# Performance work log

Measured on AMD Instinct MI355X. Metric: run time of the kernel, lower is better.

## Reference

```python
import jax, jax.numpy as jnp
import numpy as np

SEQ, B, H, NP, HN = 2048, 2, 2048, 16, 128
SCALE = 1.0 / 11.313708498984761  # 1/sqrt(128), hardcoded in the source baddbmm


def setup_inputs() -> dict:
    key = jax.random.key(0)
    k1, k2, k3 = jax.random.split(key, 3)
    return {
        "hidden_states": jax.random.normal(k1, (SEQ, B, H), dtype=jnp.float32),
        "w_qkv": jax.random.normal(k2, (3 * H, H), dtype=jnp.float32) * 0.02,
        "w_out": jax.random.normal(k3, (H, H), dtype=jnp.float32) * 0.02,
    }


def reference(hidden_states, w_qkv, w_out):
    s, b, h = hidden_states.shape
    # QKV projection (column-parallel linear, no bias): [s, b, 3h]
    qkv = hidden_states @ w_qkv.T
    # [s, b, np, 3*hn] then split (num_query_groups == num_heads)
    qkv = qkv.reshape(s, b, NP, 3 * HN)
    q, k, v = qkv[..., :HN], qkv[..., HN:2 * HN], qkv[..., 2 * HN:]
    # baddbmm QK^T with alpha = 1/sqrt(128): scores [b, np, sq, sk]
    scores = jnp.einsum("sbnh,tbnh->bnst", q, k) * SCALE
    # scale_t == 1 then plain softmax (fallback path; no mask applied)
    prob = jax.nn.softmax(scores, axis=-1)
    # context: bmm(prob, V) -> [sq, b, np, hn] -> [sq, b, h]
    ctx = jnp.einsum("bnst,tbnh->sbnh", prob, v).reshape(s, b, h)
    # row-parallel output linear (no bias)
    return ctx @ w_out.T
```

## Files before the change

### kernel.cpp

```cpp
#include <hip/hip_runtime.h>
#include <stdint.h>

#define SEQ 2048
#define BATCH 2
#define HID 2048
#define NHEADS 16
#define HDIM 128
#define QKV_LD 6144
#define SCALE_F 0.08838834764831845f
#define LOG2E_F 1.4426950408889634f

typedef unsigned short u16;
using bf16x8 = __attribute__((ext_vector_type(8))) short;
using f32x4  = __attribute__((ext_vector_type(4))) float;

__device__ inline u16 f2bf(float f) {
  union { float f; uint32_t u; } c; c.f = f;
  uint32_t u = c.u;
  uint32_t r = (u + 0x7fffu + ((u >> 16) & 1u)) >> 16;
  return (u16)r;
}

__device__ inline void gl_lds16(const u16* g, u16* l) {
  __builtin_amdgcn_global_load_lds((const __attribute__((address_space(1))) void*)g,
                                   (__attribute__((address_space(3))) void*)l,
                                   16, 0, 0);
}

__global__ void cvt_all(const float* __restrict__ hs, const float* __restrict__ wqkv,
                        const float* __restrict__ wout, u16* __restrict__ ws_out) {
  int i = blockIdx.x * blockDim.x + threadIdx.x;
  const float* src;
  int j;
  float sc = 1.0f;
  if (i < 2097152) { src = hs; j = i; }
  else if (i < 5242880) {
    j = i - 2097152; src = wqkv;
    const int f = j >> 9;
    if ((f % 384) < 128) sc = SCALE_F;
  } else { j = i - 5242880; src = wout; }
  float4 v = ((const float4*)src)[j];
  ushort4 o;
  o.x = f2bf(v.x * sc); o.y = f2bf(v.y * sc); o.z = f2bf(v.z * sc); o.w = f2bf(v.w * sc);
  ((ushort4*)ws_out)[i] = o;
}

template<int MODE>
__global__ __launch_bounds__(256)
void gemm_bt(const u16* __restrict__ A, const u16* __restrict__ Bw,
             void* __restrict__ Cout, u16* __restrict__ vt, int M, int N, int K) {
  __shared__ __align__(16) u16 As[128 * 64];
  __shared__ __align__(16) u16 Bs[128 * 64];
  const int bm = blockIdx.x, bn = blockIdx.y;
  const int tid = threadIdx.x;
  const int wave = tid >> 6, lane = tid & 63;
  const int quad = lane >> 4, l16 = lane & 15;
  const int wm = (wave >> 1) * 64, wn = (wave & 1) * 64;
  f32x4 acc[4][4] = {};

  const u16* Ablk = A + (size_t)(bm * 128) * K;
  const u16* Bblk = Bw + (size_t)(bn * 128) * K;

  for (int k0 = 0; k0 < K; k0 += 64) {
    __syncthreads();
    #pragma unroll
    for (int p = 0; p < 4; ++p) {
      int j = p * 256 + tid;
      int r = j >> 3, cs = j & 7, c = cs ^ (r & 7);
      gl_lds16(Ablk + (size_t)r * K + k0 + c * 8, As + (p * 256 + wave * 64) * 8);
      gl_lds16(Bblk + (size_t)r * K + k0 + c * 8, Bs + (p * 256 + wave * 64) * 8);
    }
    __syncthreads();
    #pragma unroll
    for (int ks = 0; ks < 2; ++ks) {
      bf16x8 af[4], bfr[4];
      #pragma unroll
      for (int mt = 0; mt < 4; ++mt) {
        int row = wm + mt * 16 + l16;
        int cc = (ks * 4 + quad) ^ (row & 7);
        af[mt] = *(const bf16x8*)&As[(row * 8 + cc) * 8];
      }
      #pragma unroll
      for (int nt = 0; nt < 4; ++nt) {
        int row = wn + nt * 16 + l16;
        int cc = (ks * 4 + quad) ^ (row & 7);
        bfr[nt] = *(const bf16x8*)&Bs[(row * 8 + cc) * 8];
      }
      #pragma unroll
      for (int mt = 0; mt < 4; ++mt)
        #pragma unroll
        for (int nt = 0; nt < 4; ++nt)
          acc[mt][nt] = __builtin_amdgcn_mfma_f32_16x16x32_bf16(af[mt], bfr[nt], acc[mt][nt], 0, 0, 0);
    }
  }

  if (MODE == 1 && (bn % 3) == 2) {
    const int h = bn / 3;
    u16* vt0 = vt + ((size_t)h * HDIM) * SEQ;
    u16* vt1 = vt + ((size_t)(NHEADS + h) * HDIM) * SEQ;
    #pragma unroll
    for (int mt = 0; mt < 4; ++mt)
      #pragma unroll
      for (int nt = 0; nt < 4; ++nt) {
        const int hd = wn + nt * 16 + l16;
        const int s0 = (bm * 128 + wm + mt * 16 + quad * 4) >> 1;
        uint32_t w0 = (uint32_t)f2bf(acc[mt][nt][0]) | ((uint32_t)f2bf(acc[mt][nt][2]) << 16);
        uint32_t w1 = (uint32_t)f2bf(acc[mt][nt][1]) | ((uint32_t)f2bf(acc[mt][nt][3]) << 16);
        *(uint32_t*)&vt0[(size_t)hd * SEQ + s0] = w0;
        *(uint32_t*)&vt1[(size_t)hd * SEQ + s0] = w1;
      }
    return;
  }

  #pragma unroll
  for (int mt = 0; mt < 4; ++mt)
    #pragma unroll
    for (int nt = 0; nt < 4; ++nt)
      #pragma unroll
      for (int r = 0; r < 4; ++r) {
        int row = bm * 128 + wm + mt * 16 + quad * 4 + r;
        int col = bn * 128 + wn + nt * 16 + l16;
        float v = acc[mt][nt][r];
        if (MODE == 1) ((u16*)Cout)[(size_t)row * N + col] = f2bf(v);
        else           ((float*)Cout)[(size_t)row * N + col] = v;
      }
}

__global__ __launch_bounds__(512, 2)
void attn(const u16* __restrict__ qkv, const u16* __restrict__ vt_g, u16* __restrict__ ctx) {
  const int qt = blockIdx.x, head = blockIdx.y, b = blockIdx.z;
  const int q0 = qt * 256;
  __shared__ __align__(16) u16 Ks[64 * 128];
  __shared__ __align__(16) u16 Vt[144 * 64];
  __shared__ __align__(16) u16 PsT[256 * 64];
  const int tid = threadIdx.x;
  const int wave = tid >> 6, lane = tid & 63;
  const int quad = lane >> 4, l16 = lane & 15;

  const u16* qkv_bh = qkv + (size_t)b * QKV_LD + head * 384;
  const u16* vt = vt_g + (size_t)(b * NHEADS + head) * HDIM * SEQ;

  if (tid < 128) {
    const int row = 128 + (tid >> 3), c = tid & 7;
    const u16 v = (row == 128) ? (u16)0x3F80 : (u16)0;
    ushort4 q4; q4.x = v; q4.y = v; q4.z = v; q4.w = v;
    *(ushort4*)&Vt[(row * 8 + c) * 8] = q4;
    *(ushort4*)&Vt[(row * 8 + c) * 8 + 4] = q4;
  }

  bf16x8 qf[2][4];
  #pragma unroll
  for (int h = 0; h < 4; ++h) {
    __syncthreads();
    #pragma unroll
    for (int p = 0; p < 2; ++p) {
      int j = p * 512 + tid;
      int r = j >> 4, cs = j & 15, c = cs ^ (r & 7);
      gl_lds16(qkv_bh + (size_t)(q0 + h * 64 + r) * (BATCH * QKV_LD) + c * 8,
               Ks + (p * 512 + wave * 64) * 8);
    }
    __syncthreads();
    if ((wave >> 1) == h) {
      #pragma unroll
      for (int nt = 0; nt < 2; ++nt)
        #pragma unroll
        for (int ks = 0; ks < 4; ++ks) {
          int row = (wave & 1) * 32 + nt * 16 + l16;
          int cc = (ks * 4 + quad) ^ (row & 7);
          qf[nt][ks] = *(const bf16x8*)&Ks[(row * 16 + cc) * 8];
        }
    }
  }

  f32x4 ot[9][2] = {};

  for (int kt = 0; kt < SEQ; kt += 64) {
    __syncthreads();
    #pragma unroll
    for (int p = 0; p < 2; ++p) {
      int j = p * 512 + tid;
      int r = j >> 4, cs = j & 15, c = cs ^ (r & 7);
      gl_lds16(qkv_bh + (size_t)(kt + r) * (BATCH * QKV_LD) + 128 + c * 8,
               Ks + (p * 512 + wave * 64) * 8);
    }
    #pragma unroll
    for (int p = 0; p < 2; ++p) {
      int j = p * 512 + tid;
      int hd = j >> 3, cs = j & 7, c = cs ^ (hd & 7);
      gl_lds16(vt + (size_t)hd * SEQ + kt + c * 8,
               Vt + (p * 512 + wave * 64) * 8);
    }
    __syncthreads();

    f32x4 st[4][2] = {};
    #pragma unroll
    for (int ks = 0; ks < 4; ++ks) {
      bf16x8 kf[4];
      #pragma unroll
      for (int mt = 0; mt < 4; ++mt) {
        int key = mt * 16 + l16;
        int cc = (ks * 4 + quad) ^ (key & 7);
        kf[mt] = *(const bf16x8*)&Ks[(key * 16 + cc) * 8];
      }
      #pragma unroll
      for (int mt = 0; mt < 4; ++mt)
        #pragma unroll
        for (int nt = 0; nt < 2; ++nt)
          st[mt][nt] = __builtin_amdgcn_mfma_f32_16x16x32_bf16(kf[mt], qf[nt][ks], st[mt][nt], 0, 0, 0);
    }

    #pragma unroll
    for (int mt = 0; mt < 4; ++mt)
      #pragma unroll
      for (int nt = 0; nt < 2; ++nt) {
        ushort4 pk;
        union { float f; uint32_t u; } cv;
        cv.f = __builtin_amdgcn_exp2f(st[mt][nt][0] * LOG2E_F); pk.x = (u16)(cv.u >> 16);
        cv.f = __builtin_amdgcn_exp2f(st[mt][nt][1] * LOG2E_F); pk.y = (u16)(cv.u >> 16);
        cv.f = __builtin_amdgcn_exp2f(st[mt][nt][2] * LOG2E_F); pk.z = (u16)(cv.u >> 16);
        cv.f = __builtin_amdgcn_exp2f(st[mt][nt][3] * LOG2E_F); pk.w = (u16)(cv.u >> 16);
        const int q = wave * 32 + nt * 16 + l16;
        const int kc = mt * 2 + (quad >> 1);
        *(ushort4*)&PsT[q * 64 + ((kc ^ (l16 & 7)) * 8 + (quad & 1) * 4)] = pk;
      }

    #pragma unroll
    for (int ks = 0; ks < 2; ++ks) {
      bf16x8 pf[2], vf[9];
      #pragma unroll
      for (int nt = 0; nt < 2; ++nt) {
        const int q = wave * 32 + nt * 16 + l16;
        const int cc = (ks * 4 + quad) ^ (l16 & 7);
        pf[nt] = *(const bf16x8*)&PsT[q * 64 + cc * 8];
      }
      #pragma unroll
      for (int mt = 0; mt < 9; ++mt) {
        const int hd = mt * 16 + l16;
        const int cc = (ks * 4 + quad) ^ (hd & 7);
        vf[mt] = *(const bf16x8*)&Vt[(hd * 8 + cc) * 8];
      }
      #pragma unroll
      for (int mt = 0; mt < 9; ++mt)
        #pragma unroll
        for (int nt = 0; nt < 2; ++nt)
          ot[mt][nt] = __builtin_amdgcn_mfma_f32_16x16x32_bf16(vf[mt], pf[nt], ot[mt][nt], 0, 0, 0);
    }
  }

  #pragma unroll
  for (int nt = 0; nt < 2; ++nt) {
    const float lv = __shfl(ot[8][nt][0], l16);
    const float inv_l = 1.0f / lv;
    const int s = q0 + wave * 32 + nt * 16 + l16;
    u16* dst = ctx + ((size_t)s * BATCH + b) * HID + head * HDIM;
    #pragma unroll
    for (int mt = 0; mt < 8; ++mt) {
      ushort4 w;
      w.x = f2bf(ot[mt][nt][0] * inv_l);
      w.y = f2bf(ot[mt][nt][1] * inv_l);
      w.z = f2bf(ot[mt][nt][2] * inv_l);
      w.w = f2bf(ot[mt][nt][3] * inv_l);
      *(ushort4*)&dst[mt * 16 + quad * 4] = w;
    }
  }
}

extern "C" void kernel_launch(void* const* d_in, const int* in_sizes, int n_in,
                              void* d_out, int out_size, void* d_ws, size_t ws_size,
                              hipStream_t stream) {
  const float* hs   = (const float*)d_in[0];
  const float* wqkv = (const float*)d_in[1];
  const float* wout = (const float*)d_in[2];
  float* out = (float*)d_out;
  char* ws = (char*)d_ws;

  u16* hs_bf   = (u16*)(ws);
  u16* wqkv_bf = (u16*)(ws + 16777216);
  u16* wout_bf = (u16*)(ws + 41943040);
  u16* qkv_bf  = (u16*)(ws + 50331648);
  u16* vt_bf   = (u16*)(ws + 100663296);
  u16* ctx_bf  = hs_bf;

  cvt_all<<<24576, 256, 0, stream>>>(hs, wqkv, wout, (u16*)ws);

  gemm_bt<1><<<dim3(32, 48), 256, 0, stream>>>(hs_bf, wqkv_bf, qkv_bf, vt_bf, 4096, 6144, 2048);

  attn<<<dim3(8, NHEADS, BATCH), 512, 0, stream>>>(qkv_bf, vt_bf, ctx_bf);

  gemm_bt<0><<<dim3(32, 16), 256, 0, stream>>>(ctx_bf, wout_bf, out, nullptr, 4096, 2048, 2048);
}
```

Measured before the change: 382.7 us.

## Triple-buffer GEMM LDS tiles with 128x256 blocks and 512 threads

Rewrites the bf16 GEMM to use 128x256 output tiles with 8 waves and a three-stage LDS ring. Global-to-LDS loads are issued two k-steps ahead and guarded by vmcnt waits, so each iteration needs one barrier instead of two. MFMA priority is raised with s_setprio. The change aims to hide global load latency and improve B-operand reuse. In exchange it uses about 144KB of LDS per block, which limits occupancy, and with half as many blocks per launch it may underfill the CUs.

Result: slower. 410.5 us (+7.3%).

```diff
diff --git a/kernel.cpp b/kernel.cpp
--- a/kernel.cpp
+++ b/kernel.cpp
@@ -45,32 +45,54 @@
   ((ushort4*)ws_out)[i] = o;
 }
 
+__device__ __forceinline__ void stage_tile(const u16* __restrict__ Ablk,
+                                           const u16* __restrict__ Bblk,
+                                           int K, int k0, u16* As, u16* Bs,
+                                           int tid, int wave) {
+  #pragma unroll
+  for (int p = 0; p < 2; ++p) {
+    int j = p * 512 + tid;
+    int r = j >> 3, cs = j & 7, c = cs ^ (r & 7);
+    gl_lds16(Ablk + (size_t)r * K + k0 + c * 8, As + (size_t)(p * 512 + wave * 64) * 8);
+  }
+  #pragma unroll
+  for (int p = 0; p < 4; ++p) {
+    int j = p * 512 + tid;
+    int r = j >> 3, cs = j & 7, c = cs ^ (r & 7);
+    gl_lds16(Bblk + (size_t)r * K + k0 + c * 8, Bs + (size_t)(p * 512 + wave * 64) * 8);
+  }
+}
+
 template<int MODE>
-__global__ __launch_bounds__(256)
+__global__ __launch_bounds__(512)
 void gemm_bt(const u16* __restrict__ A, const u16* __restrict__ Bw,
              void* __restrict__ Cout, u16* __restrict__ vt, int M, int N, int K) {
-  __shared__ __align__(16) u16 As[128 * 64];
-  __shared__ __align__(16) u16 Bs[128 * 64];
+  __shared__ __align__(16) u16 As[3][128 * 64];
+  __shared__ __align__(16) u16 Bs[3][256 * 64];
   const int bm = blockIdx.x, bn = blockIdx.y;
   const int tid = threadIdx.x;
   const int wave = tid >> 6, lane = tid & 63;
   const int quad = lane >> 4, l16 = lane & 15;
-  const int wm = (wave >> 1) * 64, wn = (wave & 1) * 64;
+  const int wm = (wave >> 2) * 64, wn = (wave & 3) * 64;
   f32x4 acc[4][4] = {};
 
   const u16* Ablk = A + (size_t)(bm * 128) * K;
-  const u16* Bblk = Bw + (size_t)(bn * 128) * K;
-
-  for (int k0 = 0; k0 < K; k0 += 64) {
-    __syncthreads();
-    #pragma unroll
-    for (int p = 0; p < 4; ++p) {
-      int j = p * 256 + tid;
-      int r = j >> 3, cs = j & 7, c = cs ^ (r & 7);
-      gl_lds16(Ablk + (size_t)r * K + k0 + c * 8, As + (p * 256 + wave * 64) * 8);
-      gl_lds16(Bblk + (size_t)r * K + k0 + c * 8, Bs + (p * 256 + wave * 64) * 8);
-    }
-    __syncthreads();
+  const u16* Bblk = Bw + (size_t)(bn * 256) * K;
+  const int nt = K >> 6;
+
+  stage_tile(Ablk, Bblk, K, 0,  As[0], Bs[0], tid, wave);
+  stage_tile(Ablk, Bblk, K, 64, As[1], Bs[1], tid, wave);
+  asm volatile("s_waitcnt vmcnt(6)" ::: "memory");
+  __builtin_amdgcn_s_barrier();
+
+  for (int t = 0; t < nt; ++t) {
+    const int cur = t % 3;
+    if (t + 2 < nt) {
+      const int nb = (t + 2) % 3;
+      stage_tile(Ablk, Bblk, K, (t + 2) * 64, As[nb], Bs[nb], tid, wave);
+    }
+    const u16* Asb = As[cur];
+    const u16* Bsb = Bs[cur];
     #pragma unroll
     for (int ks = 0; ks < 2; ++ks) {
       bf16x8 af[4], bfr[4];
@@ -78,51 +100,68 @@
       for (int mt = 0; mt < 4; ++mt) {
         int row = wm + mt * 16 + l16;
         int cc = (ks * 4 + quad) ^ (row & 7);
-        af[mt] = *(const bf16x8*)&As[(row * 8 + cc) * 8];
-      }
-      #pragma unroll
-      for (int nt = 0; nt < 4; ++nt) {
-        int row = wn + nt * 16 + l16;
+        af[mt] = *(const bf16x8*)&Asb[(row * 8 + cc) * 8];
+      }
+      #pragma unroll
+      for (int nt2 = 0; nt2 < 4; ++nt2) {
+        int row = wn + nt2 * 16 + l16;
         int cc = (ks * 4 + quad) ^ (row & 7);
-        bfr[nt] = *(const bf16x8*)&Bs[(row * 8 + cc) * 8];
-      }
+        bfr[nt2] = *(const bf16x8*)&Bsb[(row * 8 + cc) * 8];
+      }
+      __builtin_amdgcn_s_setprio(1);
       #pragma unroll
       for (int mt = 0; mt < 4; ++mt)
         #pragma unroll
-        for (int nt = 0; nt < 4; ++nt)
-          acc[mt][nt] = __builtin_amdgcn_mfma_f32_16x16x32_bf16(af[mt], bfr[nt], acc[mt][nt], 0, 0, 0);
-    }
-  }
-
-  if (MODE == 1 && (bn % 3) == 2) {
-    const int h = bn / 3;
-    u16* vt0 = vt + ((size_t)h * HDIM) * SEQ;
-    u16* vt1 = vt + ((size_t)(NHEADS + h) * HDIM) * SEQ;
+        for (int nt2 = 0; nt2 < 4; ++nt2)
+          acc[mt][nt2] = __builtin_amdgcn_mfma_f32_16x16x32_bf16(af[mt], bfr[nt2], acc[mt][nt2], 0, 0, 0);
+      __builtin_amdgcn_s_setprio(0);
+    }
+    if (t + 2 < nt) asm volatile("s_waitcnt vmcnt(6)" ::: "memory");
+    else            asm volatile("s_waitcnt vmcnt(0)" ::: "memory");
+    __builtin_amdgcn_s_barrier();
+  }
+
+  if (MODE == 1) {
+    #pragma unroll
+    for (int ntf = 0; ntf < 4; ++ntf) {
+      const int coff = wn + ntf * 16;
+      const int g = bn * 2 + (coff >> 7);
+      const int h = g / 3;
+      if ((g % 3) == 2) {
+        const int hd = (coff & 127) + l16;
+        u16* vt0 = vt + ((size_t)h * HDIM) * SEQ;
+        u16* vt1 = vt + ((size_t)(NHEADS + h) * HDIM) * SEQ;
+        #pragma unroll
+        for (int mt = 0; mt < 4; ++mt) {
+          const int s0 = (bm * 128 + wm + mt * 16 + quad * 4) >> 1;
+          uint32_t w0 = (uint32_t)f2bf(acc[mt][ntf][0]) | ((uint32_t)f2bf(acc[mt][ntf][2]) << 16);
+          uint32_t w1 = (uint32_t)f2bf(acc[mt][ntf][1]) | ((uint32_t)f2bf(acc[mt][ntf][3]) << 16);
+          *(uint32_t*)&vt0[(size_t)hd * SEQ + s0] = w0;
+          *(uint32_t*)&vt1[(size_t)hd * SEQ + s0] = w1;
+        }
+      } else {
+        const int col = bn * 256 + coff + l16;
+        #pragma unroll
+        for (int mt = 0; mt < 4; ++mt)
+          #pragma unroll
+          for (int r = 0; r < 4; ++r) {
+            const int row = bm * 128 + wm + mt * 16 + quad * 4 + r;
+            ((u16*)Cout)[(size_t)row * N + col] = f2bf(acc[mt][ntf][r]);
+          }
+      }
+    }
+    return;
+  }
+
+  #pragma unroll
+  for (int ntf = 0; ntf < 4; ++ntf)
     #pragma unroll
     for (int mt = 0; mt < 4; ++mt)
       #pragma unroll
-      for (int nt = 0; nt < 4; ++nt) {
-        const int hd = wn + nt * 16 + l16;
-        const int s0 = (bm * 128 + wm + mt * 16 + quad * 4) >> 1;
-        uint32_t w0 = (uint32_t)f2bf(acc[mt][nt][0]) | ((uint32_t)f2bf(acc[mt][nt][2]) << 16);
-        uint32_t w1 = (uint32_t)f2bf(acc[mt][nt][1]) | ((uint32_t)f2bf(acc[mt][nt][3]) << 16);
-        *(uint32_t*)&vt0[(size_t)hd * SEQ + s0] = w0;
-        *(uint32_t*)&vt1[(size_t)hd * SEQ + s0] = w1;
-      }
-    return;
-  }
-
-  #pragma unroll
-  for (int mt = 0; mt < 4; ++mt)
-    #pragma unroll
-    for (int nt = 0; nt < 4; ++nt)
-      #pragma unroll
       for (int r = 0; r < 4; ++r) {
-        int row = bm * 128 + wm + mt * 16 + quad * 4 + r;
-        int col = bn * 128 + wn + nt * 16 + l16;
-        float v = acc[mt][nt][r];
-        if (MODE == 1) ((u16*)Cout)[(size_t)row * N + col] = f2bf(v);
-        else           ((float*)Cout)[(size_t)row * N + col] = v;
+        const int row = bm * 128 + wm + mt * 16 + quad * 4 + r;
+        const int col = bn * 256 + wn + ntf * 16 + l16;
+        ((float*)Cout)[(size_t)row * N + col] = acc[mt][ntf][r];
       }
 }
 
@@ -283,9 +322,9 @@
 
   cvt_all<<<24576, 256, 0, stream>>>(hs, wqkv, wout, (u16*)ws);
 
-  gemm_bt<1><<<dim3(32, 48), 256, 0, stream>>>(hs_bf, wqkv_bf, qkv_bf, vt_bf, 4096, 6144, 2048);
+  gemm_bt<1><<<dim3(32, 24), 512, 0, stream>>>(hs_bf, wqkv_bf, qkv_bf, vt_bf, 4096, 6144, 2048);
 
   attn<<<dim3(8, NHEADS, BATCH), 512, 0, stream>>>(qkv_bf, vt_bf, ctx_bf);
 
-  gemm_bt<0><<<dim3(32, 16), 256, 0, stream>>>(ctx_bf, wout_bf, out, nullptr, 4096, 2048, 2048);
-}
+  gemm_bt<0><<<dim3(32, 8), 512, 0, stream>>>(ctx_bf, wout_bf, out, nullptr, 4096, 2048, 2048);
+}
```

## Replace QKV GEMM with double-buffered 256x256-tile kernel with interleaved prefetch

Applied to the files above, without the earlier changes.

Adds a dedicated QKV projection kernel that uses 256x256 output tiles with 8 waves, double-buffered LDS filled by direct global-to-LDS loads, and prefetches interleaved with MFMA phases using explicit vmcnt waits, barriers and setprio. The goal is to hide global load latency and raise per-block data reuse compared with the old unpipelined 128x128 kernel. The V-transpose epilogue moves into the new kernel and is resolved per 64-column chunk, and the old MODE 1 path is dropped from gemm_bt. The cost is more LDS (128KB per block) and more registers, which lowers occupancy, plus fragile hand-tuned wait counts.

Result: slower. 429.4 us (+12.2%).

```diff
diff --git a/kernel.cpp b/kernel.cpp
--- a/kernel.cpp
+++ b/kernel.cpp
@@ -45,12 +45,178 @@
   ((ushort4*)ws_out)[i] = o;
 }
 
+#define QK_M 4096
+#define QK_N 6144
+#define QK_K 2048
+#define QK_T (QK_K / 64)
+
+__global__ __launch_bounds__(512, 2)
+void gemm256_qkv(const u16* __restrict__ A, const u16* __restrict__ Bw,
+                 u16* __restrict__ Cout, u16* __restrict__ vt) {
+  __shared__ __align__(16) u16 As[2][16384];
+  __shared__ __align__(16) u16 Bs[2][16384];
+  const int bm = blockIdx.x, bn = blockIdx.y;
+  const int tid = threadIdx.x;
+  const int wave = tid >> 6, lane = tid & 63;
+  const int quad = lane >> 4, l16 = lane & 15;
+  const int wm = (wave >> 2) * 128, wn = (wave & 3) * 64;
+  f32x4 acc[8][4] = {};
+
+  const u16* Ablk = A + (size_t)(bm * 256) * QK_K;
+  const u16* Bblk = Bw + (size_t)(bn * 256) * QK_K;
+
+  auto stageA = [&](int t, int ks, int buf) {
+    #pragma unroll
+    for (int p = 0; p < 2; ++p) {
+      int j = p * 512 + tid;
+      int row = ((j >> 6) << 4) + (j & 15);
+      int c = (j >> 4) & 3;
+      gl_lds16(Ablk + (size_t)row * QK_K + t * 64 + ks * 32 + c * 8,
+               &As[buf][ks * 8192 + (p * 512 + wave * 64) * 8]);
+    }
+  };
+  auto stageB = [&](int t, int ks, int buf) {
+    #pragma unroll
+    for (int p = 0; p < 2; ++p) {
+      int j = p * 512 + tid;
+      int row = ((j >> 6) << 4) + (j & 15);
+      int c = (j >> 4) & 3;
+      gl_lds16(Bblk + (size_t)row * QK_K + t * 64 + ks * 32 + c * 8,
+               &Bs[buf][ks * 8192 + (p * 512 + wave * 64) * 8]);
+    }
+  };
+
+  stageA(0, 0, 0); stageB(0, 0, 0);
+  stageA(0, 1, 0); stageB(0, 1, 0);
+  stageA(1, 0, 1); stageB(1, 0, 1);
+  asm volatile("s_waitcnt vmcnt(8)" ::: "memory");
+  __builtin_amdgcn_s_barrier();
+  __builtin_amdgcn_sched_barrier(0);
+
+  for (int t = 0; t < QK_T; ++t) {
+    const int cb = t & 1;
+    const u16* Ab = &As[cb][0];
+    const u16* Bb = &Bs[cb][0];
+    bf16x8 af[4], bfr[4];
+
+    #pragma unroll
+    for (int mt = 0; mt < 4; ++mt) {
+      int row = wm + mt * 16 + l16;
+      af[mt] = *(const bf16x8*)&Ab[(((row >> 4) << 6) + quad * 16 + (row & 15)) * 8];
+    }
+    #pragma unroll
+    for (int nt = 0; nt < 4; ++nt) {
+      int row = wn + nt * 16 + l16;
+      bfr[nt] = *(const bf16x8*)&Bb[(((row >> 4) << 6) + quad * 16 + (row & 15)) * 8];
+    }
+    if (t + 1 < QK_T) stageA(t + 1, 1, cb ^ 1);
+    __builtin_amdgcn_s_barrier();
+    __builtin_amdgcn_s_setprio(1);
+    #pragma unroll
+    for (int mt = 0; mt < 4; ++mt)
+      #pragma unroll
+      for (int nt = 0; nt < 4; ++nt)
+        acc[mt][nt] = __builtin_amdgcn_mfma_f32_16x16x32_bf16(af[mt], bfr[nt], acc[mt][nt], 0, 0, 0);
+    __builtin_amdgcn_s_setprio(0);
+    __builtin_amdgcn_s_barrier();
+
+    #pragma unroll
+    for (int mt = 0; mt < 4; ++mt) {
+      int row = wm + 64 + mt * 16 + l16;
+      af[mt] = *(const bf16x8*)&Ab[(((row >> 4) << 6) + quad * 16 + (row & 15)) * 8];
+    }
+    if (t + 1 < QK_T) stageB(t + 1, 1, cb ^ 1);
+    __builtin_amdgcn_s_barrier();
+    __builtin_amdgcn_s_setprio(1);
+    #pragma unroll
+    for (int mt = 0; mt < 4; ++mt)
+      #pragma unroll
+      for (int nt = 0; nt < 4; ++nt)
+        acc[4 + mt][nt] = __builtin_amdgcn_mfma_f32_16x16x32_bf16(af[mt], bfr[nt], acc[4 + mt][nt], 0, 0, 0);
+    __builtin_amdgcn_s_setprio(0);
+    if (t < QK_T - 1) asm volatile("s_waitcnt vmcnt(8)" ::: "memory");
+    else              asm volatile("s_waitcnt vmcnt(0)" ::: "memory");
+    __builtin_amdgcn_s_barrier();
+    __builtin_amdgcn_sched_barrier(0);
+
+    #pragma unroll
+    for (int mt = 0; mt < 4; ++mt) {
+      int row = wm + mt * 16 + l16;
+      af[mt] = *(const bf16x8*)&Ab[8192 + (((row >> 4) << 6) + quad * 16 + (row & 15)) * 8];
+    }
+    #pragma unroll
+    for (int nt = 0; nt < 4; ++nt) {
+      int row = wn + nt * 16 + l16;
+      bfr[nt] = *(const bf16x8*)&Bb[8192 + (((row >> 4) << 6) + quad * 16 + (row & 15)) * 8];
+    }
+    if (t + 2 < QK_T) stageA(t + 2, 0, cb);
+    __builtin_amdgcn_s_barrier();
+    __builtin_amdgcn_s_setprio(1);
+    #pragma unroll
+    for (int mt = 0; mt < 4; ++mt)
+      #pragma unroll
+      for (int nt = 0; nt < 4; ++nt)
+        acc[mt][nt] = __builtin_amdgcn_mfma_f32_16x16x32_bf16(af[mt], bfr[nt], acc[mt][nt], 0, 0, 0);
+    __builtin_amdgcn_s_setprio(0);
+    __builtin_amdgcn_s_barrier();
+
+    #pragma unroll
+    for (int mt = 0; mt < 4; ++mt) {
+      int row = wm + 64 + mt * 16 + l16;
+      af[mt] = *(const bf16x8*)&Ab[8192 + (((row >> 4) << 6) + quad * 16 + (row & 15)) * 8];
+    }
+    if (t + 2 < QK_T) stageB(t + 2, 0, cb);
+    __builtin_amdgcn_s_barrier();
+    __builtin_amdgcn_s_setprio(1);
+    #pragma unroll
+    for (int mt = 0; mt < 4; ++mt)
+      #pragma unroll
+      for (int nt = 0; nt < 4; ++nt)
+        acc[4 + mt][nt] = __builtin_amdgcn_mfma_f32_16x16x32_bf16(af[mt], bfr[nt], acc[4 + mt][nt], 0, 0, 0);
+    __builtin_amdgcn_s_setprio(0);
+    if (t < QK_T - 2)       asm volatile("s_waitcnt vmcnt(8)" ::: "memory");
+    else if (t == QK_T - 2) asm volatile("s_waitcnt vmcnt(4)" ::: "memory");
+    else                    asm volatile("s_waitcnt vmcnt(0)" ::: "memory");
+    __builtin_amdgcn_s_barrier();
+    __builtin_amdgcn_sched_barrier(0);
+  }
+
+  #pragma unroll
+  for (int ntf = 0; ntf < 4; ++ntf) {
+    const int coff = wn + ntf * 16;
+    const int g = bn * 2 + (coff >> 7);
+    const int h = g / 3;
+    if ((g % 3) == 2) {
+      const int hd = (coff & 127) + l16;
+      u16* vt0 = vt + ((size_t)h * HDIM) * SEQ;
+      u16* vt1 = vt + ((size_t)(NHEADS + h) * HDIM) * SEQ;
+      #pragma unroll
+      for (int mt = 0; mt < 8; ++mt) {
+        const int s0 = (bm * 256 + wm + mt * 16 + quad * 4) >> 1;
+        uint32_t w0 = (uint32_t)f2bf(acc[mt][ntf][0]) | ((uint32_t)f2bf(acc[mt][ntf][2]) << 16);
+        uint32_t w1 = (uint32_t)f2bf(acc[mt][ntf][1]) | ((uint32_t)f2bf(acc[mt][ntf][3]) << 16);
+        *(uint32_t*)&vt0[(size_t)hd * SEQ + s0] = w0;
+        *(uint32_t*)&vt1[(size_t)hd * SEQ + s0] = w1;
+      }
+    } else {
+      const int col = bn * 256 + coff + l16;
+      #pragma unroll
+      for (int mt = 0; mt < 8; ++mt)
+        #pragma unroll
+        for (int r = 0; r < 4; ++r) {
+          const int row = bm * 256 + wm + mt * 16 + quad * 4 + r;
+          Cout[(size_t)row * QK_N + col] = f2bf(acc[mt][ntf][r]);
+        }
+    }
+  }
+}
+
 template<int MODE>
 __global__ __launch_bounds__(256)
 void gemm_bt(const u16* __restrict__ A, const u16* __restrict__ Bw,
              void* __restrict__ Cout, u16* __restrict__ vt, int M, int N, int K) {
-  __shared__ __align__(16) u16 As[128 * 64];
-  __shared__ __align__(16) u16 Bs[128 * 64];
+  __shared__ __align__(16) u16 Asx[128 * 64];
+  __shared__ __align__(16) u16 Bsx[128 * 64];
   const int bm = blockIdx.x, bn = blockIdx.y;
   const int tid = threadIdx.x;
   const int wave = tid >> 6, lane = tid & 63;
@@ -67,8 +233,8 @@
     for (int p = 0; p < 4; ++p) {
       int j = p * 256 + tid;
       int r = j >> 3, cs = j & 7, c = cs ^ (r & 7);
-      gl_lds16(Ablk + (size_t)r * K + k0 + c * 8, As + (p * 256 + wave * 64) * 8);
-      gl_lds16(Bblk + (size_t)r * K + k0 + c * 8, Bs + (p * 256 + wave * 64) * 8);
+      gl_lds16(Ablk + (size_t)r * K + k0 + c * 8, Asx + (p * 256 + wave * 64) * 8);
+      gl_lds16(Bblk + (size_t)r * K + k0 + c * 8, Bsx + (p * 256 + wave * 64) * 8);
     }
     __syncthreads();
     #pragma unroll
@@ -78,13 +244,13 @@
       for (int mt = 0; mt < 4; ++mt) {
         int row = wm + mt * 16 + l16;
         int cc = (ks * 4 + quad) ^ (row & 7);
-        af[mt] = *(const bf16x8*)&As[(row * 8 + cc) * 8];
+        af[mt] = *(const bf16x8*)&Asx[(row * 8 + cc) * 8];
       }
       #pragma unroll
       for (int nt = 0; nt < 4; ++nt) {
         int row = wn + nt * 16 + l16;
         int cc = (ks * 4 + quad) ^ (row & 7);
-        bfr[nt] = *(const bf16x8*)&Bs[(row * 8 + cc) * 8];
+        bfr[nt] = *(const bf16x8*)&Bsx[(row * 8 + cc) * 8];
       }
       #pragma unroll
       for (int mt = 0; mt < 4; ++mt)
@@ -92,24 +258,6 @@
         for (int nt = 0; nt < 4; ++nt)
           acc[mt][nt] = __builtin_amdgcn_mfma_f32_16x16x32_bf16(af[mt], bfr[nt], acc[mt][nt], 0, 0, 0);
     }
-  }
-
-  if (MODE == 1 && (bn % 3) == 2) {
-    const int h = bn / 3;
-    u16* vt0 = vt + ((size_t)h * HDIM) * SEQ;
-    u16* vt1 = vt + ((size_t)(NHEADS + h) * HDIM) * SEQ;
-    #pragma unroll
-    for (int mt = 0; mt < 4; ++mt)
-      #pragma unroll
-      for (int nt = 0; nt < 4; ++nt) {
-        const int hd = wn + nt * 16 + l16;
-        const int s0 = (bm * 128 + wm + mt * 16 + quad * 4) >> 1;
-        uint32_t w0 = (uint32_t)f2bf(acc[mt][nt][0]) | ((uint32_t)f2bf(acc[mt][nt][2]) << 16);
-        uint32_t w1 = (uint32_t)f2bf(acc[mt][nt][1]) | ((uint32_t)f2bf(acc[mt][nt][3]) << 16);
-        *(uint32_t*)&vt0[(size_t)hd * SEQ + s0] = w0;
-        *(uint32_t*)&vt1[(size_t)hd * SEQ + s0] = w1;
-      }
-    return;
   }
 
   #pragma unroll
@@ -283,7 +431,7 @@
 
   cvt_all<<<24576, 256, 0, stream>>>(hs, wqkv, wout, (u16*)ws);
 
-  gemm_bt<1><<<dim3(32, 48), 256, 0, stream>>>(hs_bf, wqkv_bf, qkv_bf, vt_bf, 4096, 6144, 2048);
+  gemm256_qkv<<<dim3(16, 24), 512, 0, stream>>>(hs_bf, wqkv_bf, qkv_bf, vt_bf);
 
   attn<<<dim3(8, NHEADS, BATCH), 512, 0, stream>>>(qkv_bf, vt_bf, ctx_bf);
 
```

## Double-buffer K/V tiles in attention and raise MFMA wave priority

Applied to the files above, without the earlier changes.

The attention kernel now keeps two LDS buffers for the K and transposed-V tiles. It issues the async global-to-LDS loads for the next 64-key tile before computing on the current one, which replaces the two barriers per iteration with one trailing barrier. This is meant to hide global load latency behind the QK^T, exp and PV MFMA work. The MFMA blocks are also wrapped in s_setprio raises. LDS use grows to about 100KB per block, which may prevent two blocks sharing a CU. With this grid size that is likely not a binding limit.

Measured after the change: 365.1 us (median of 3 runs). -4.6%, faster.

```diff
diff --git a/kernel.cpp b/kernel.cpp
--- a/kernel.cpp
+++ b/kernel.cpp
@@ -130,8 +130,8 @@
 void attn(const u16* __restrict__ qkv, const u16* __restrict__ vt_g, u16* __restrict__ ctx) {
   const int qt = blockIdx.x, head = blockIdx.y, b = blockIdx.z;
   const int q0 = qt * 256;
-  __shared__ __align__(16) u16 Ks[64 * 128];
-  __shared__ __align__(16) u16 Vt[144 * 64];
+  __shared__ __align__(16) u16 Ks[2][64 * 128];
+  __shared__ __align__(16) u16 Vt[2][144 * 64];
   __shared__ __align__(16) u16 PsT[256 * 64];
   const int tid = threadIdx.x;
   const int wave = tid >> 6, lane = tid & 63;
@@ -144,8 +144,11 @@
     const int row = 128 + (tid >> 3), c = tid & 7;
     const u16 v = (row == 128) ? (u16)0x3F80 : (u16)0;
     ushort4 q4; q4.x = v; q4.y = v; q4.z = v; q4.w = v;
-    *(ushort4*)&Vt[(row * 8 + c) * 8] = q4;
-    *(ushort4*)&Vt[(row * 8 + c) * 8 + 4] = q4;
+    #pragma unroll
+    for (int bb = 0; bb < 2; ++bb) {
+      *(ushort4*)&Vt[bb][(row * 8 + c) * 8] = q4;
+      *(ushort4*)&Vt[bb][(row * 8 + c) * 8 + 4] = q4;
+    }
   }
 
   bf16x8 qf[2][4];
@@ -157,7 +160,7 @@
       int j = p * 512 + tid;
       int r = j >> 4, cs = j & 15, c = cs ^ (r & 7);
       gl_lds16(qkv_bh + (size_t)(q0 + h * 64 + r) * (BATCH * QKV_LD) + c * 8,
-               Ks + (p * 512 + wave * 64) * 8);
+               Ks[0] + (p * 512 + wave * 64) * 8);
     }
     __syncthreads();
     if ((wave >> 1) == h) {
@@ -167,30 +170,39 @@
         for (int ks = 0; ks < 4; ++ks) {
           int row = (wave & 1) * 32 + nt * 16 + l16;
           int cc = (ks * 4 + quad) ^ (row & 7);
-          qf[nt][ks] = *(const bf16x8*)&Ks[(row * 16 + cc) * 8];
+          qf[nt][ks] = *(const bf16x8*)&Ks[0][(row * 16 + cc) * 8];
         }
     }
   }
 
-  f32x4 ot[9][2] = {};
-
-  for (int kt = 0; kt < SEQ; kt += 64) {
-    __syncthreads();
+  auto stageKV = [&](int kt, int bb) {
     #pragma unroll
     for (int p = 0; p < 2; ++p) {
       int j = p * 512 + tid;
       int r = j >> 4, cs = j & 15, c = cs ^ (r & 7);
       gl_lds16(qkv_bh + (size_t)(kt + r) * (BATCH * QKV_LD) + 128 + c * 8,
-               Ks + (p * 512 + wave * 64) * 8);
+               Ks[bb] + (p * 512 + wave * 64) * 8);
     }
     #pragma unroll
     for (int p = 0; p < 2; ++p) {
       int j = p * 512 + tid;
       int hd = j >> 3, cs = j & 7, c = cs ^ (hd & 7);
       gl_lds16(vt + (size_t)hd * SEQ + kt + c * 8,
-               Vt + (p * 512 + wave * 64) * 8);
-    }
-    __syncthreads();
+               Vt[bb] + (p * 512 + wave * 64) * 8);
+    }
+  };
+
+  f32x4 ot[9][2] = {};
+
+  __syncthreads();
+  stageKV(0, 0);
+  __syncthreads();
+
+  for (int it = 0; it < SEQ / 64; ++it) {
+    const int cur = it & 1;
+    if (it + 1 < SEQ / 64) stageKV((it + 1) * 64, cur ^ 1);
+    const u16* Kb = Ks[cur];
+    const u16* Vb = Vt[cur];
 
     f32x4 st[4][2] = {};
     #pragma unroll
@@ -200,13 +212,15 @@
       for (int mt = 0; mt < 4; ++mt) {
         int key = mt * 16 + l16;
         int cc = (ks * 4 + quad) ^ (key & 7);
-        kf[mt] = *(const bf16x8*)&Ks[(key * 16 + cc) * 8];
-      }
+        kf[mt] = *(const bf16x8*)&Kb[(key * 16 + cc) * 8];
+      }
+      __builtin_amdgcn_s_setprio(1);
       #pragma unroll
       for (int mt = 0; mt < 4; ++mt)
         #pragma unroll
         for (int nt = 0; nt < 2; ++nt)
           st[mt][nt] = __builtin_amdgcn_mfma_f32_16x16x32_bf16(kf[mt], qf[nt][ks], st[mt][nt], 0, 0, 0);
+      __builtin_amdgcn_s_setprio(0);
     }
 
     #pragma unroll
@@ -237,14 +251,18 @@
       for (int mt = 0; mt < 9; ++mt) {
         const int hd = mt * 16 + l16;
         const int cc = (ks * 4 + quad) ^ (hd & 7);
-        vf[mt] = *(const bf16x8*)&Vt[(hd * 8 + cc) * 8];
-      }
+        vf[mt] = *(const bf16x8*)&Vb[(hd * 8 + cc) * 8];
+      }
+      __builtin_amdgcn_s_setprio(1);
       #pragma unroll
       for (int mt = 0; mt < 9; ++mt)
         #pragma unroll
         for (int nt = 0; nt < 2; ++nt)
           ot[mt][nt] = __builtin_amdgcn_mfma_f32_16x16x32_bf16(vf[mt], pf[nt], ot[mt][nt], 0, 0, 0);
-    }
+      __builtin_amdgcn_s_setprio(0);
+    }
+
+    __syncthreads();
   }
 
   #pragma unroll
```
